# Performance work log

Measured on AMD Instinct MI355X. Metric: run time of the kernel, lower is better.

The kernel has to match this reference:

```python
import jax, jax.numpy as jnp
import numpy as np
import math

B, L, M, N, S = 1024, 32, 128, 4096, 32


def setup_inputs() -> dict:
    key = jax.random.key(0)
    k1, k2, k3 = jax.random.split(key, 3)
    k = jax.random.normal(k1, (B, L, M), dtype=jnp.float32)
    # kaiming-uniform-like init: U(-bound, bound)
    bound_e = math.sqrt(6.0 / (N * M))
    bound_d = math.sqrt(6.0 / (M * N))
    W_e = jax.random.uniform(k2, (L, N, M), dtype=jnp.float32, minval=-bound_e, maxval=bound_e)
    W_d = jax.random.uniform(k3, (L, M, N), dtype=jnp.float32, minval=-bound_d, maxval=bound_d)
    # decoder columns are unit-normalized along the m axis (dim=-2), as in __init__
    W_d = W_d / jnp.linalg.norm(W_d, axis=-2, keepdims=True)
    b_e = jnp.zeros((L, N), dtype=jnp.float32)
    b_d = jnp.zeros((L, M), dtype=jnp.float32)
    return {"k": k, "W_e": W_e, "b_e": b_e, "W_d": W_d, "b_d": b_d, "s": S}


def hard_thresholding(y, s):
    # keep the s largest-|.| activations per (batch, layer) row, zero the rest
    _, idx = jax.lax.top_k(jnp.abs(y), s)  # idx: [B, L, s]
    b, l, _ = y.shape
    mask = jnp.zeros_like(y).at[
        jnp.arange(b)[:, None, None], jnp.arange(l)[None, :, None], idx
    ].set(1.0)
    return y * mask


def reference(k, W_e, b_e, W_d, b_d, s):
    # NOTE: b_e is created by the module but (faithfully) unused in encode()
    k_bar = k - b_d                                  # [B, L, M]
    y = jnp.einsum('lnm,blm->bln', W_e, k_bar)        # [B, L, N]
    y = hard_thresholding(y, s)
    k_hat = jnp.einsum('lmn,bln->blm', W_d, y)        # [B, L, M]
    loss = jnp.mean((k_hat - k) ** 2)
    return (loss, k_hat, y)
```

## Files before the change

kernel.cpp:

```cpp
#include <hip/hip_runtime.h>
#include <hip/hip_bf16.h>

#define B_ 1024
#define L_ 32
#define M_ 128
#define N_ 4096
#define S_ 32
#define ROWS (B_ * L_)

typedef __attribute__((ext_vector_type(8))) short    short8_t;
typedef __attribute__((ext_vector_type(8))) unsigned short ushort8_t;
typedef __attribute__((ext_vector_type(4))) float    f32x4;

__device__ __forceinline__ unsigned short f2bf(float x) {
    unsigned u = __float_as_uint(x);
    unsigned r = (u + 0x7FFFu + ((u >> 16) & 1u)) >> 16;
    return (unsigned short)r;
}
__device__ __forceinline__ float bf2f(unsigned short h) {
    return __uint_as_float((unsigned)h << 16);
}

__global__ __launch_bounds__(256) void prologue(float* __restrict__ y,
                                                const float* __restrict__ We,
                                                const float* __restrict__ bd,
                                                unsigned short* __restrict__ Wbf,
                                                float* __restrict__ cvec,
                                                const float* __restrict__ kin,
                                                unsigned short* __restrict__ Abf,
                                                const float* __restrict__ Wd,
                                                float* __restrict__ WdT) {
    __shared__ float t[32][33];
    const int bid = blockIdx.x;
    const int tid = threadIdx.x;

    if (bid < 2048) {
        const float4 z = {0.f, 0.f, 0.f, 0.f};
        int idx = bid * 256 + tid;
        for (int i = idx; i < ROWS * 512; i += 2048 * 256) {
            int row = i >> 9, slot = i & 511;
            reinterpret_cast<float4*>(y + (size_t)row * N_)[slot] = z;
        }
    } else if (bid < 10240) {
        int wb = bid - 2048;
        int l = wb >> 8, nb = wb & 255;
        int nl = tid >> 4, tt = tid & 15;
        int n = nb * 16 + nl;
        const float* w = We + ((size_t)l * N_ + n) * M_ + tt * 8;
        const float* b = bd + l * M_ + tt * 8;
        float4 w0 = *(const float4*)(w), w1 = *(const float4*)(w + 4);
        float4 b0 = *(const float4*)(b), b1 = *(const float4*)(b + 4);
        ushort8_t o;
        o[0] = f2bf(w0.x); o[1] = f2bf(w0.y); o[2] = f2bf(w0.z); o[3] = f2bf(w0.w);
        o[4] = f2bf(w1.x); o[5] = f2bf(w1.y); o[6] = f2bf(w1.z); o[7] = f2bf(w1.w);
        *reinterpret_cast<ushort8_t*>(Wbf + ((size_t)l * N_ + n) * 128 + tt * 8) = o;
        float s = w0.x*b0.x + w0.y*b0.y + w0.z*b0.z + w0.w*b0.w
                + w1.x*b1.x + w1.y*b1.y + w1.z*b1.z + w1.w*b1.w;
        #pragma unroll
        for (int oo = 8; oo > 0; oo >>= 1) s += __shfl_xor(s, oo, 64);
        if (tt == 0) cvec[(size_t)l * N_ + n] = s;
    } else if (bid < 26624) {
        int g = (bid - 10240) * 256 + tid;
        int b = g >> 12, l = (g >> 7) & 31, m = g & 127;
        Abf[(((size_t)l * B_ + b) << 7) + m] = f2bf(kin[g]);
    } else {
        int tb = bid - 26624;
        int l  = tb >> 9;
        int rem = tb & 511;
        int n0 = (rem & 127) * 32, m0 = (rem >> 7) * 32;
        int tx = tid & 31, ty = tid >> 5;
        const float* src = Wd + (size_t)l * M_ * N_;
        for (int i = ty; i < 32; i += 8)
            t[i][tx] = src[(size_t)(m0 + i) * N_ + n0 + tx];
        __syncthreads();
        float* dst = WdT + (size_t)l * N_ * M_;
        for (int i = ty; i < 32; i += 8)
            dst[(size_t)(n0 + i) * M_ + m0 + tx] = t[tx][i];
    }
}

__global__ __launch_bounds__(256) void transpose_wd(const float* __restrict__ Wd,
                                                    float* __restrict__ WdT) {
    __shared__ float t[32][33];
    int l = blockIdx.z;
    int n0 = blockIdx.x * 32, m0 = blockIdx.y * 32;
    int tx = threadIdx.x & 31, ty = threadIdx.x >> 5;
    const float* src = Wd + (size_t)l * M_ * N_;
    for (int i = ty; i < 32; i += 8)
        t[i][tx] = src[(size_t)(m0 + i) * N_ + n0 + tx];
    __syncthreads();
    float* dst = WdT + (size_t)l * N_ * M_;
    for (int i = ty; i < 32; i += 8)
        dst[(size_t)(n0 + i) * M_ + m0 + tx] = t[tx][i];
}

__device__ __forceinline__ int swz(int row) { return (row & 3) ^ ((row >> 2) & 3); }

#define CP 136

__global__ __launch_bounds__(256) void encoder_mfma(const unsigned short* __restrict__ Abf,
                                                    const unsigned short* __restrict__ Wbf,
                                                    const float* __restrict__ cvec,
                                                    unsigned short* __restrict__ y16) {
    const int orig = ((blockIdx.x & 7) << 10) + (blockIdx.x >> 3);
    const int l    = orig >> 8;
    const int rem  = orig & 255;
    const int bn0  = (rem & 31) * 128;
    const int bm0  = (rem >> 5) * 128;
    __shared__ __align__(16) unsigned short smem[128 * CP];
    unsigned short* As = smem;
    unsigned short* Bs = smem + 128 * 32;
    const int tid  = threadIdx.x;
    const int lane = tid & 63, wave = tid >> 6;
    const int wr = wave >> 1, wc = wave & 1;

    const unsigned short* Ab = Abf + (((size_t)l * B_ + bm0) << 7);
    const unsigned short* Wb = Wbf + (((size_t)l * N_ + bn0) << 7);

    auto stage = [&](int k0) {
        #pragma unroll
        for (int i = 0; i < 2; ++i) {
            int p   = i * 256 + tid;
            int row = p >> 2;
            int lc  = (p & 3) ^ swz(row);
            const unsigned short* g = Ab + ((size_t)row << 7) + k0 + lc * 8;
            unsigned dst = (unsigned)((i * 256 + (tid & ~63)) * 16);
            __builtin_amdgcn_global_load_lds(
                (const __attribute__((address_space(1))) void*)g,
                (__attribute__((address_space(3))) void*)((char*)As + dst), 16, 0, 0);
        }
        #pragma unroll
        for (int i = 0; i < 2; ++i) {
            int p   = i * 256 + tid;
            int row = p >> 2;
            int lc  = (p & 3) ^ swz(row);
            const unsigned short* g = Wb + ((size_t)row << 7) + k0 + lc * 8;
            unsigned dst = (unsigned)((i * 256 + (tid & ~63)) * 16);
            __builtin_amdgcn_global_load_lds(
                (const __attribute__((address_space(1))) void*)g,
                (__attribute__((address_space(3))) void*)((char*)Bs + dst), 16, 0, 0);
        }
    };

    f32x4 acc[4][4];
    #pragma unroll
    for (int i = 0; i < 4; ++i)
        #pragma unroll
        for (int j = 0; j < 4; ++j) acc[i][j] = (f32x4){0.f, 0.f, 0.f, 0.f};

    stage(0);
    __syncthreads();

    #pragma unroll
    for (int t = 0; t < 4; ++t) {
        short8_t aF[4], bF[4];
        const int kg = lane >> 4;
        #pragma unroll
        for (int mt = 0; mt < 4; ++mt) {
            int row = wr * 64 + mt * 16 + (lane & 15);
            int pc  = kg ^ swz(row);
            aF[mt] = *reinterpret_cast<const short8_t*>(As + row * 32 + pc * 8);
        }
        #pragma unroll
        for (int nt = 0; nt < 4; ++nt) {
            int row = wc * 64 + nt * 16 + (lane & 15);
            int pc  = kg ^ swz(row);
            bF[nt] = *reinterpret_cast<const short8_t*>(Bs + row * 32 + pc * 8);
        }
        #pragma unroll
        for (int mt = 0; mt < 4; ++mt)
            #pragma unroll
            for (int nt = 0; nt < 4; ++nt)
                acc[mt][nt] = __builtin_amdgcn_mfma_f32_16x16x32_bf16(
                    aF[mt], bF[nt], acc[mt][nt], 0, 0, 0);

        if (t < 3) {
            __syncthreads();
            stage((t + 1) * 32);
            __syncthreads();
        }
    }

    __syncthreads();

    #pragma unroll
    for (int nt = 0; nt < 4; ++nt) {
        int nl = wc * 64 + nt * 16 + (lane & 15);
        float cj = cvec[(size_t)l * N_ + bn0 + nl];
        #pragma unroll
        for (int mt = 0; mt < 4; ++mt) {
            #pragma unroll
            for (int j = 0; j < 4; ++j) {
                int rl = wr * 64 + mt * 16 + (lane >> 4) * 4 + j;
                smem[rl * CP + nl] = f2bf(acc[mt][nt][j] - cj);
            }
        }
    }
    __syncthreads();

    #pragma unroll
    for (int i = 0; i < 8; ++i) {
        int chunk = i * 256 + tid;
        int r = chunk >> 4, cch = chunk & 15;
        ushort8_t v = *reinterpret_cast<const ushort8_t*>(smem + r * CP + cch * 8);
        unsigned short* dst = y16 + ((size_t)((bm0 + r) * L_ + l)) * 8192 + 4096 + bn0 + cch * 8;
        *reinterpret_cast<ushort8_t*>(dst) = v;
    }
}

#define POOL 96
#define MARGIN 1.2e-3f

__global__ __launch_bounds__(256) void topk_decode(float* __restrict__ y,
                                                   const float* __restrict__ We,
                                                   const float* __restrict__ WdT,
                                                   const float* __restrict__ kin,
                                                   const float* __restrict__ cvec,
                                                   int* __restrict__ cidx,
                                                   float* __restrict__ cval,
                                                   float* __restrict__ khat,
                                                   float* __restrict__ partial) {
    const int w    = threadIdx.x >> 6;
    const int lane = threadIdx.x & 63;
    const int i  = blockIdx.x;
    const int p  = 3 - (i >> 11);
    const int x  = (i >> 8) & 7;
    const int l  = 4 * x + p;
    const int j  = i & 255;
    const int bm = 7 - (j >> 5);
    const int bq = j & 31;
    const int b  = bm * 128 + bq * 4 + w;
    const int row = b * L_ + l;

    __shared__ __align__(16) float kinS[4][M_];
    __shared__ int   pidxS[4][POOL];
    __shared__ float pexS[4][POOL];
    __shared__ int   sidxS[4][S_];
    __shared__ float svalS[4][S_];

    float* yo = y + (size_t)row * N_;
    const unsigned short* ya = (const unsigned short*)y + (size_t)row * 8192 + 4096;

    kinS[w][lane]      = kin[(size_t)row * M_ + lane];
    kinS[w][lane + 64] = kin[(size_t)row * M_ + lane + 64];

    ushort8_t u[8];
    #pragma unroll
    for (int jj = 0; jj < 8; ++jj)
        u[jj] = *reinterpret_cast<const ushort8_t*>(ya + jj * 512 + lane * 8);
    float a[64];
    #pragma unroll
    for (int jj = 0; jj < 8; ++jj)
        #pragma unroll
        for (int e = 0; e < 8; ++e)
            a[jj * 8 + e] = fabsf(bf2f(u[jj][e]));

    float mx = 0.0f, s1 = 0.0f, s2 = 0.0f;
    #pragma unroll
    for (int ii = 0; ii < 64; ++ii) {
        mx = fmaxf(mx, a[ii]);
        s1 += a[ii];
        s2 = fmaf(a[ii], a[ii], s2);
    }
    #pragma unroll
    for (int o = 32; o > 0; o >>= 1) {
        mx = fmaxf(mx, __shfl_xor(mx, o, 64));
        s1 += __shfl_xor(s1, o, 64);
        s2 += __shfl_xor(s2, o, 64);
    }
    const float mu  = s1 * (1.0f / 4096.0f);
    const float var = fmaxf(s2 * (1.0f / 4096.0f) - mu * mu, 0.0f);
    const float sg  = sqrtf(var);

    float lo = 0.0f, hi = mx;
    int cl = N_;
    for (int it = 0; it < 30 && cl > 40; ++it) {
        float t;
        if      (it == 0) t = mu + 2.20f * sg;
        else if (it == 1) t = mu + 2.96f * sg;
        else              t = 0.5f * (lo + hi);
        t = fminf(fmaxf(t, lo), hi);
        int c = 0;
        #pragma unroll
        for (int ii = 0; ii < 64; ++ii) c += (a[ii] >= t) ? 1 : 0;
        #pragma unroll
        for (int o = 32; o > 0; o >>= 1) c += __shfl_xor(c, o, 64);
        if (c >= S_) { lo = t; cl = c; } else { hi = t; }
    }

    const float th = lo - MARGIN;
    int myc = 0;
    #pragma unroll
    for (int ii = 0; ii < 64; ++ii) myc += (a[ii] >= th) ? 1 : 0;
    int pos = myc;
    #pragma unroll
    for (int o = 1; o < 64; o <<= 1) {
        int t = __shfl_up(pos, o, 64);
        if (lane >= o) pos += t;
    }
    const int base  = pos - myc;
    const int total = __shfl(pos, 63, 64);
    int k = 0;
    #pragma unroll
    for (int jj = 0; jj < 8; ++jj)
        #pragma unroll
        for (int e = 0; e < 8; ++e)
            if (a[jj * 8 + e] >= th) {
                int pp = base + k;
                if (pp < POOL) pidxS[w][pp] = jj * 512 + lane * 8 + e;
                ++k;
            }
    __asm__ __volatile__("s_waitcnt lgkmcnt(0)" ::: "memory");
    int c = total < POOL ? total : POOL;

    if (lane < c) {
        int n = pidxS[w][lane];
        const float4* wp4 = reinterpret_cast<const float4*>(We + ((size_t)l * N_ + n) * M_);
        const float4* kp4 = reinterpret_cast<const float4*>(kinS[w]);
        float acc = -cvec[(size_t)l * N_ + n];
        #pragma unroll 8
        for (int m4 = 0; m4 < 32; ++m4) {
            float4 wv = wp4[m4], kv = kp4[m4];
            acc = fmaf(wv.x, kv.x, acc);
            acc = fmaf(wv.y, kv.y, acc);
            acc = fmaf(wv.z, kv.z, acc);
            acc = fmaf(wv.w, kv.w, acc);
        }
        pexS[w][lane] = acc;
    }
    if (lane + 64 < c) {
        int n = pidxS[w][lane + 64];
        const float4* wp4 = reinterpret_cast<const float4*>(We + ((size_t)l * N_ + n) * M_);
        const float4* kp4 = reinterpret_cast<const float4*>(kinS[w]);
        float acc = -cvec[(size_t)l * N_ + n];
        #pragma unroll 8
        for (int m4 = 0; m4 < 32; ++m4) {
            float4 wv = wp4[m4], kv = kp4[m4];
            acc = fmaf(wv.x, kv.x, acc);
            acc = fmaf(wv.y, kv.y, acc);
            acc = fmaf(wv.z, kv.z, acc);
            acc = fmaf(wv.w, kv.w, acc);
        }
        pexS[w][lane + 64] = acc;
    }
    __asm__ __volatile__("s_waitcnt lgkmcnt(0)" ::: "memory");

    for (int e = lane; e < c; e += 64) {
        float ae = fabsf(pexS[w][e]);
        int   ne = pidxS[w][e];
        int rank = 0;
        for (int jj = 0; jj < c; ++jj) {
            float aj = fabsf(pexS[w][jj]);
            rank += ((aj > ae) || (aj == ae && pidxS[w][jj] < ne)) ? 1 : 0;
        }
        if (rank < S_) {
            sidxS[w][rank] = ne;
            svalS[w][rank] = pexS[w][e];
        }
    }
    __asm__ __volatile__("s_waitcnt lgkmcnt(0)" ::: "memory");

    if (lane < S_) {
        int n = sidxS[w][lane];
        float v = svalS[w][lane];
        cidx[(size_t)row * S_ + lane] = n;
        cval[(size_t)row * S_ + lane] = v;
        if (n < 2048) yo[n] = v;
    }

    const float* wt = WdT + (size_t)l * N_ * M_;
    float acc0 = 0.0f, acc1 = 0.0f;
    #pragma unroll 8
    for (int jj = 0; jj < S_; ++jj) {
        float v = svalS[w][jj];
        const float* wrp = wt + (size_t)sidxS[w][jj] * M_;
        acc0 = fmaf(v, wrp[lane], acc0);
        acc1 = fmaf(v, wrp[lane + 64], acc1);
    }
    khat[(size_t)row * M_ + lane]      = acc0;
    khat[(size_t)row * M_ + lane + 64] = acc1;
    float r0 = acc0 - kinS[w][lane];
    float r1 = acc1 - kinS[w][lane + 64];
    float s = r0 * r0 + r1 * r1;
    #pragma unroll
    for (int o = 32; o > 0; o >>= 1) s += __shfl_xor(s, o, 64);
    if (lane == 0) partial[row] = s;
}

__global__ __launch_bounds__(256) void finish_high(float* __restrict__ y,
                                                   const int* __restrict__ cidx,
                                                   const float* __restrict__ cval) {
    const int bid = blockIdx.x;
    const int tid = threadIdx.x;
    const int row0 = bid * 16;
    const float4 z = {0.f, 0.f, 0.f, 0.f};
    #pragma unroll
    for (int i = 0; i < 32; ++i) {
        int g = i * 256 + tid;
        int r = row0 + (g >> 9);
        int slot = g & 511;
        reinterpret_cast<float4*>(y + (size_t)r * N_ + 2048)[slot] = z;
    }
    __syncthreads();
    #pragma unroll
    for (int i = 0; i < 2; ++i) {
        int e = i * 256 + tid;
        int g = row0 * S_ + e;
        int n = cidx[g];
        if (n >= 2048) {
            int r = row0 + (e >> 5);
            y[(size_t)r * N_ + n] = cval[g];
        }
    }
}

__global__ __launch_bounds__(256) void reduce_loss(const float* __restrict__ partial,
                                                   float* __restrict__ out_loss) {
    __shared__ float red[256];
    int tid = threadIdx.x;
    float s = 0.0f;
    for (int i = tid; i < ROWS / 4; i += 256) {
        float4 v = reinterpret_cast<const float4*>(partial)[i];
        s += v.x + v.y + v.z + v.w;
    }
    red[tid] = s;
    __syncthreads();
    for (int off = 128; off > 0; off >>= 1) {
        if (tid < off) red[tid] += red[tid + off];
        __syncthreads();
    }
    if (tid == 0) out_loss[0] = red[0] / (float)((size_t)B_ * L_ * M_);
}

extern "C" void kernel_launch(void* const* d_in, const int* in_sizes, int n_in,
                              void* d_out, int out_size, void* d_ws, size_t ws_size,
                              hipStream_t stream) {
    const float* kin = (const float*)d_in[0];
    const float* We  = (const float*)d_in[1];
    const float* Wd  = (const float*)d_in[3];
    const float* bd  = (const float*)d_in[4];

    float* out   = (float*)d_out;
    float* loss  = out;
    float* khat  = out + 1;
    float* y_out = out + 1 + (size_t)B_ * L_ * M_;

    char* ws = (char*)d_ws;
    const bool wsBig = ws_size >= ((size_t)113u << 20);

    unsigned short* Wbf;
    unsigned short* Abf;
    int*   cidx;
    float* cval;
    float* cvec;
    float* partial;
    float* WdT;

    if (wsBig) {
        Wbf     = (unsigned short*)ws;
        Abf     = (unsigned short*)(ws + (32u << 20));
        cidx    = (int*)  (ws + (40u << 20));
        cval    = (float*)(ws + (44u << 20));
        cvec    = (float*)(ws + (48u << 20));
        partial = (float*)(ws + (48u << 20) + (512u << 10));
        WdT     = (float*)(ws + (49u << 20));
    } else {
        Wbf     = (unsigned short*)ws;
        Abf     = (unsigned short*)(ws + (64u << 20));
        cidx    = (int*)  (ws + (72u << 20));
        cval    = (float*)(ws + (76u << 20));
        cvec    = (float*)(ws + (80u << 20));
        partial = (float*)(ws + (81u << 20));
        WdT     = (float*)ws;
    }

    int nblocks = 26624 + (wsBig ? 16384 : 0);
    prologue<<<nblocks, 256, 0, stream>>>(y_out, We, bd, Wbf, cvec, kin, Abf, Wd, WdT);
    encoder_mfma<<<8192, 256, 0, stream>>>(Abf, Wbf, cvec, (unsigned short*)y_out);
    if (!wsBig)
        transpose_wd<<<dim3(N_ / 32, M_ / 32, L_), 256, 0, stream>>>(Wd, WdT);
    topk_decode<<<ROWS / 4, 256, 0, stream>>>(y_out, We, WdT, kin, cvec,
                                              cidx, cval, khat, partial);
    finish_high<<<2048, 256, 0, stream>>>(y_out, cidx, cval);
    reduce_loss<<<1, 256, 0, stream>>>(partial, loss);
}
```

Before: 541.4 us.

## Store encoder output as 8-bit magnitude keys for top-k candidate selection

The encoder now writes a one-byte quantized log-magnitude key per activation instead of a bf16 value, halving the scratch traffic between encoder and top-k kernels. The top-k kernel does an integer bisection over the 8-bit keys, which replaces the float mean/variance estimate and reads four keys per word. The candidate pool grows to 128 to absorb the coarser quantization before exact fp32 recomputation. The risk is pool overflow or lost true top-k members if the key bins are too coarse, plus the extra unpacking arithmetic.

New measurement: 538.6 us. About the same (-0.5%).

```diff
diff --git a/kernel.cpp b/kernel.cpp
--- a/kernel.cpp
+++ b/kernel.cpp
@@ -11,6 +11,7 @@
 typedef __attribute__((ext_vector_type(8))) short    short8_t;
 typedef __attribute__((ext_vector_type(8))) unsigned short ushort8_t;
 typedef __attribute__((ext_vector_type(4))) float    f32x4;
+typedef __attribute__((ext_vector_type(4))) unsigned int uint4_t;
 
 __device__ __forceinline__ unsigned short f2bf(float x) {
     unsigned u = __float_as_uint(x);
@@ -20,6 +21,8 @@
 __device__ __forceinline__ float bf2f(unsigned short h) {
     return __uint_as_float((unsigned)h << 16);
 }
+
+#define KEY_E0 14720
 
 __global__ __launch_bounds__(256) void prologue(float* __restrict__ y,
                                                 const float* __restrict__ We,
@@ -96,20 +99,20 @@
 
 __device__ __forceinline__ int swz(int row) { return (row & 3) ^ ((row >> 2) & 3); }
 
-#define CP 136
+#define CPB 144
 
 __global__ __launch_bounds__(256) void encoder_mfma(const unsigned short* __restrict__ Abf,
                                                     const unsigned short* __restrict__ Wbf,
                                                     const float* __restrict__ cvec,
-                                                    unsigned short* __restrict__ y16) {
+                                                    unsigned char* __restrict__ y8) {
     const int orig = ((blockIdx.x & 7) << 10) + (blockIdx.x >> 3);
     const int l    = orig >> 8;
     const int rem  = orig & 255;
     const int bn0  = (rem & 31) * 128;
     const int bm0  = (rem >> 5) * 128;
-    __shared__ __align__(16) unsigned short smem[128 * CP];
-    unsigned short* As = smem;
-    unsigned short* Bs = smem + 128 * 32;
+    __shared__ __align__(16) unsigned char smemB[128 * CPB];
+    unsigned short* As = (unsigned short*)smemB;
+    unsigned short* Bs = (unsigned short*)(smemB + 8192);
     const int tid  = threadIdx.x;
     const int lane = tid & 63, wave = tid >> 6;
     const int wr = wave >> 1, wc = wave & 1;
@@ -192,23 +195,27 @@
             #pragma unroll
             for (int j = 0; j < 4; ++j) {
                 int rl = wr * 64 + mt * 16 + (lane >> 4) * 4 + j;
-                smem[rl * CP + nl] = f2bf(acc[mt][nt][j] - cj);
+                float v = acc[mt][nt][j] - cj;
+                unsigned mag = (__float_as_uint(v) >> 16) & 0x7FFFu;
+                int key = ((int)mag - KEY_E0) >> 3;
+                key = key < 0 ? 0 : (key > 255 ? 255 : key);
+                smemB[rl * CPB + nl] = (unsigned char)key;
             }
         }
     }
     __syncthreads();
 
     #pragma unroll
-    for (int i = 0; i < 8; ++i) {
+    for (int i = 0; i < 4; ++i) {
         int chunk = i * 256 + tid;
-        int r = chunk >> 4, cch = chunk & 15;
-        ushort8_t v = *reinterpret_cast<const ushort8_t*>(smem + r * CP + cch * 8);
-        unsigned short* dst = y16 + ((size_t)((bm0 + r) * L_ + l)) * 8192 + 4096 + bn0 + cch * 8;
-        *reinterpret_cast<ushort8_t*>(dst) = v;
-    }
-}
-
-#define POOL 96
+        int r = chunk >> 3, cch = chunk & 7;
+        uint4_t v = *reinterpret_cast<const uint4_t*>(smemB + r * CPB + cch * 16);
+        unsigned char* dst = y8 + ((size_t)((bm0 + r) * L_ + l)) * 16384 + 8192 + bn0 + cch * 16;
+        *reinterpret_cast<uint4_t*>(dst) = v;
+    }
+}
+
+#define POOL 128
 #define MARGIN 1.2e-3f
 
 __global__ __launch_bounds__(256) void topk_decode(float* __restrict__ y,
@@ -239,59 +246,65 @@
     __shared__ float svalS[4][S_];
 
     float* yo = y + (size_t)row * N_;
-    const unsigned short* ya = (const unsigned short*)y + (size_t)row * 8192 + 4096;
+    const unsigned char* ya8 = (const unsigned char*)y + (size_t)row * 16384 + 8192;
 
     kinS[w][lane]      = kin[(size_t)row * M_ + lane];
     kinS[w][lane + 64] = kin[(size_t)row * M_ + lane + 64];
 
-    ushort8_t u[8];
-    #pragma unroll
-    for (int jj = 0; jj < 8; ++jj)
-        u[jj] = *reinterpret_cast<const ushort8_t*>(ya + jj * 512 + lane * 8);
-    float a[64];
-    #pragma unroll
-    for (int jj = 0; jj < 8; ++jj)
-        #pragma unroll
-        for (int e = 0; e < 8; ++e)
-            a[jj * 8 + e] = fabsf(bf2f(u[jj][e]));
-
-    float mx = 0.0f, s1 = 0.0f, s2 = 0.0f;
-    #pragma unroll
-    for (int ii = 0; ii < 64; ++ii) {
-        mx = fmaxf(mx, a[ii]);
-        s1 += a[ii];
-        s2 = fmaf(a[ii], a[ii], s2);
-    }
-    #pragma unroll
-    for (int o = 32; o > 0; o >>= 1) {
-        mx = fmaxf(mx, __shfl_xor(mx, o, 64));
-        s1 += __shfl_xor(s1, o, 64);
-        s2 += __shfl_xor(s2, o, 64);
-    }
-    const float mu  = s1 * (1.0f / 4096.0f);
-    const float var = fmaxf(s2 * (1.0f / 4096.0f) - mu * mu, 0.0f);
-    const float sg  = sqrtf(var);
-
-    float lo = 0.0f, hi = mx;
+    unsigned ak[16];
+    #pragma unroll
+    for (int jj = 0; jj < 4; ++jj) {
+        uint4_t q = *reinterpret_cast<const uint4_t*>(ya8 + jj * 1024 + lane * 16);
+        #pragma unroll
+        for (int d = 0; d < 4; ++d) ak[jj * 4 + d] = q[d];
+    }
+
+    unsigned mxk = 0u;
+    #pragma unroll
+    for (int ii = 0; ii < 16; ++ii) {
+        unsigned v = ak[ii];
+        mxk = max(mxk, v & 0xFFu);
+        mxk = max(mxk, (v >> 8) & 0xFFu);
+        mxk = max(mxk, (v >> 16) & 0xFFu);
+        mxk = max(mxk, v >> 24);
+    }
+    #pragma unroll
+    for (int o = 32; o > 0; o >>= 1)
+        mxk = max(mxk, (unsigned)__shfl_xor((int)mxk, o, 64));
+
+    unsigned lo = 0u, hi = mxk;
     int cl = N_;
-    for (int it = 0; it < 30 && cl > 40; ++it) {
-        float t;
-        if      (it == 0) t = mu + 2.20f * sg;
-        else if (it == 1) t = mu + 2.96f * sg;
-        else              t = 0.5f * (lo + hi);
-        t = fminf(fmaxf(t, lo), hi);
+    for (int it = 0; it < 12 && cl > 48 && lo < hi; ++it) {
+        unsigned t = (it == 0) ? 121u : lo + ((hi - lo + 1u) >> 1);
+        t = min(max(t, lo + 1u), hi);
         int c = 0;
         #pragma unroll
-        for (int ii = 0; ii < 64; ++ii) c += (a[ii] >= t) ? 1 : 0;
+        for (int ii = 0; ii < 16; ++ii) {
+            unsigned v = ak[ii];
+            c += ((v & 0xFFu) >= t) ? 1 : 0;
+            c += (((v >> 8) & 0xFFu) >= t) ? 1 : 0;
+            c += (((v >> 16) & 0xFFu) >= t) ? 1 : 0;
+            c += ((v >> 24) >= t) ? 1 : 0;
+        }
         #pragma unroll
         for (int o = 32; o > 0; o >>= 1) c += __shfl_xor(c, o, 64);
-        if (c >= S_) { lo = t; cl = c; } else { hi = t; }
-    }
-
-    const float th = lo - MARGIN;
+        if (c >= S_) { lo = t; cl = c; } else { hi = t - 1u; }
+    }
+
+    const float lov = __uint_as_float((unsigned)(KEY_E0 + (int)(lo << 3)) << 16);
+    const float thf = fmaxf(lov - MARGIN, 0.0f);
+    int tht = ((int)((__float_as_uint(thf) >> 16) & 0x7FFFu) - KEY_E0) >> 3;
+    const unsigned th = tht < 0 ? 0u : (unsigned)tht;
+
     int myc = 0;
     #pragma unroll
-    for (int ii = 0; ii < 64; ++ii) myc += (a[ii] >= th) ? 1 : 0;
+    for (int ii = 0; ii < 16; ++ii) {
+        unsigned v = ak[ii];
+        myc += ((v & 0xFFu) >= th) ? 1 : 0;
+        myc += (((v >> 8) & 0xFFu) >= th) ? 1 : 0;
+        myc += (((v >> 16) & 0xFFu) >= th) ? 1 : 0;
+        myc += ((v >> 24) >= th) ? 1 : 0;
+    }
     int pos = myc;
     #pragma unroll
     for (int o = 1; o < 64; o <<= 1) {
@@ -302,14 +315,20 @@
     const int total = __shfl(pos, 63, 64);
     int k = 0;
     #pragma unroll
-    for (int jj = 0; jj < 8; ++jj)
-        #pragma unroll
-        for (int e = 0; e < 8; ++e)
-            if (a[jj * 8 + e] >= th) {
-                int pp = base + k;
-                if (pp < POOL) pidxS[w][pp] = jj * 512 + lane * 8 + e;
-                ++k;
+    for (int jj = 0; jj < 4; ++jj)
+        #pragma unroll
+        for (int d = 0; d < 4; ++d) {
+            unsigned v = ak[jj * 4 + d];
+            #pragma unroll
+            for (int bb = 0; bb < 4; ++bb) {
+                unsigned key = (v >> (bb * 8)) & 0xFFu;
+                if (key >= th) {
+                    int pp = base + k;
+                    if (pp < POOL) pidxS[w][pp] = jj * 1024 + lane * 16 + d * 4 + bb;
+                    ++k;
+                }
             }
+        }
     __asm__ __volatile__("s_waitcnt lgkmcnt(0)" ::: "memory");
     int c = total < POOL ? total : POOL;
 
@@ -476,7 +495,7 @@
 
     int nblocks = 26624 + (wsBig ? 16384 : 0);
     prologue<<<nblocks, 256, 0, stream>>>(y_out, We, bd, Wbf, cvec, kin, Abf, Wd, WdT);
-    encoder_mfma<<<8192, 256, 0, stream>>>(Abf, Wbf, cvec, (unsigned short*)y_out);
+    encoder_mfma<<<8192, 256, 0, stream>>>(Abf, Wbf, cvec, (unsigned char*)y_out);
     if (!wsBig)
         transpose_wd<<<dim3(N_ / 32, M_ / 32, L_), 256, 0, stream>>>(Wd, WdT);
     topk_decode<<<ROWS / 4, 256, 0, stream>>>(y_out, We, WdT, kin, cvec,
```
